# Kernel tuning notes

Hardware: AMD Instinct MI355X
Metric: run time of the kernel (lower is better)

The kernel has to match this reference:

```python
import jax, jax.numpy as jnp
import numpy as np

N_NODES = 100000
N_EDGES = 1600000
IN, HID, OUT = 128, 128, 64


def setup_inputs() -> dict:
    key = jax.random.key(0)
    ks = jax.random.split(key, 12)
    x = jax.random.normal(ks[0], (N_NODES, IN), dtype=jnp.float32)
    src = jax.random.randint(ks[1], (N_EDGES,), 0, N_NODES, dtype=jnp.int32)
    dst = jax.random.randint(ks[2], (N_EDGES,), 0, N_NODES, dtype=jnp.int32)
    def lin(k, fan_in, fan_out):
        s = 1.0 / np.sqrt(fan_in)
        return (jax.random.normal(k, (fan_in, fan_out), dtype=jnp.float32) * s)
    dims = [(IN, HID), (HID, HID), (HID, OUT)]
    params = {}
    for l, (fi, fo) in enumerate(dims):
        params[f"Wself{l}"] = lin(ks[3 + 3 * l], fi, fo)
        params[f"Wneigh{l}"] = lin(ks[4 + 3 * l], fi, fo)
        params[f"b{l}"] = jnp.zeros((fo,), dtype=jnp.float32)
    return {"x": x, "src": src, "dst": dst, **params}


def _sage_conv(h, src, dst, inv_deg, Ws, Wn, b):
    # mean aggregation over in-neighbors: segment-sum of gathered src feats / degree
    agg = jax.ops.segment_sum(h[src], dst, num_segments=N_NODES) * inv_deg
    return h @ Ws + agg @ Wn + b


def reference(x, src, dst, Wself0, Wneigh0, b0, Wself1, Wneigh1, b1, Wself2, Wneigh2, b2):
    deg = jax.ops.segment_sum(jnp.ones((N_EDGES,), jnp.float32), dst, num_segments=N_NODES)
    inv_deg = (1.0 / jnp.maximum(deg, 1.0))[:, None]  # zero-degree nodes get zero agg
    h = jax.nn.relu(_sage_conv(x, src, dst, inv_deg, Wself0, Wneigh0, b0))
    h = jax.nn.relu(_sage_conv(h, src, dst, inv_deg, Wself1, Wneigh1, b1))
    h = _sage_conv(h, src, dst, inv_deg, Wself2, Wneigh2, b2)
    return h
```

## Files before the change

kernel.cpp:

```cpp
#include <hip/hip_runtime.h>
#include <hip/hip_bf16.h>

#define N_NODES 100000
#define N_EDGES 1600000
#define BSHIFT 8
#define NB 391
#define BCAP 8192

typedef __attribute__((ext_vector_type(8))) short short8;
typedef __attribute__((ext_vector_type(4))) float f32x4;
typedef unsigned short ushort;
typedef unsigned int uint;

__device__ __forceinline__ ushort f2bf(float f) {
    uint u = __float_as_uint(f);
    uint r = (u + 0x7fffu + ((u >> 16) & 1u)) >> 16;
    return (ushort)r;
}
__device__ __forceinline__ float bflo(uint v) { return __uint_as_float(v << 16); }
__device__ __forceinline__ float bfhi(uint v) { return __uint_as_float(v & 0xffff0000u); }


__global__ __launch_bounds__(256) void partA_kernel(const int* __restrict__ src,
                                                    const int* __restrict__ dst,
                                                    uint* __restrict__ packed,
                                                    int* __restrict__ bucket_cnt, int E) {
    constexpr int PER = 16;
    __shared__ int cnt[NB];
    __shared__ int cur[NB];
    int tid = threadIdx.x;
    for (int i = tid; i < NB; i += 256) cnt[i] = 0;
    __syncthreads();
    int base = blockIdx.x * (256 * PER);
    int d[PER], s[PER];
#pragma unroll
    for (int i = 0; i < PER; i++) {
        int e = base + tid + i * 256;
        if (e < E) {
            d[i] = dst[e];
            s[i] = src[e];
            atomicAdd(&cnt[d[i] >> BSHIFT], 1);
        } else {
            d[i] = -1;
        }
    }
    __syncthreads();
    for (int i = tid; i < NB; i += 256) cur[i] = atomicAdd(&bucket_cnt[i], cnt[i]);
    __syncthreads();
#pragma unroll
    for (int i = 0; i < PER; i++) {
        if (d[i] >= 0) {
            int b = d[i] >> BSHIFT;
            int p = atomicAdd(&cur[b], 1);
            packed[(size_t)b * BCAP + p] = ((uint)(d[i] & 255) << 17) | (uint)s[i];
        }
    }
}


__global__ __launch_bounds__(256) void partB_kernel(const uint* __restrict__ packed,
                                                    const int* __restrict__ bucket_cnt,
                                                    int* __restrict__ row_ptr,
                                                    float* __restrict__ inv_deg,
                                                    int* __restrict__ col, int N, int E) {
    __shared__ int deg[256];
    __shared__ int cur[256];
    __shared__ int psum[256];
    __shared__ int sofs;
    int b = blockIdx.x, tid = threadIdx.x;
    int cnt = bucket_cnt[b];
    {
        int part = 0;
        for (int i = tid; i < b; i += 256) part += bucket_cnt[i];
        psum[tid] = part;
        __syncthreads();
        for (int off = 128; off > 0; off >>= 1) {
            if (tid < off) psum[tid] += psum[tid + off];
            __syncthreads();
        }
        if (tid == 0) sofs = psum[0];
        __syncthreads();
    }
    int bofs = sofs;
    const uint* pk = packed + (size_t)b * BCAP;
    deg[tid] = 0;
    __syncthreads();
    for (int e = tid; e < cnt; e += 1024) {
        uint w[4];
        int have[4];
#pragma unroll
        for (int j = 0; j < 4; j++) {
            int ee = e + j * 256;
            have[j] = ee < cnt;
            w[j] = pk[have[j] ? ee : e];
        }
#pragma unroll
        for (int j = 0; j < 4; j++)
            if (have[j]) atomicAdd(&deg[w[j] >> 17], 1);
    }
    __syncthreads();
    int d0 = deg[tid];
    psum[tid] = d0;
    __syncthreads();
    for (int off = 1; off < 256; off <<= 1) {
        int x = psum[tid];
        int y = (tid >= off) ? psum[tid - off] : 0;
        __syncthreads();
        psum[tid] = x + y;
        __syncthreads();
    }
    int excl = psum[tid] - d0;
    cur[tid] = excl;
    int g = (b << BSHIFT) + tid;
    if (g < N) {
        row_ptr[g] = bofs + excl;
        inv_deg[g] = 1.0f / (float)(d0 > 1 ? d0 : 1);
    }
    if (b == 0 && tid == 0) row_ptr[N] = E;
    __syncthreads();
    for (int e = tid; e < cnt; e += 1024) {
        uint w[4];
        int have[4];
#pragma unroll
        for (int j = 0; j < 4; j++) {
            int ee = e + j * 256;
            have[j] = ee < cnt;
            w[j] = pk[have[j] ? ee : e];
        }
#pragma unroll
        for (int j = 0; j < 4; j++)
            if (have[j]) {
                int dl = w[j] >> 17;
                int p = atomicAdd(&cur[dl], 1);
                col[bofs + p] = (int)(w[j] & 0x1FFFFu);
            }
    }
}


#define CAST_BLK 6250

__global__ __launch_bounds__(256) void prep_kernel(const float* __restrict__ x,
                                                   ushort* __restrict__ xb,
                                                   const float* __restrict__ Ws0,
                                                   const float* __restrict__ Wn0,
                                                   const float* __restrict__ Ws1,
                                                   const float* __restrict__ Wn1,
                                                   const float* __restrict__ Ws2,
                                                   const float* __restrict__ Wn2,
                                                   ushort* __restrict__ BT0,
                                                   ushort* __restrict__ BT1,
                                                   ushort* __restrict__ BT2) {
    int blk = blockIdx.x;
    if (blk < CAST_BLK) {
        long n8 = (long)N_NODES * 128 / 8;
        long g = (long)blk * 256 + threadIdx.x;
        if (g >= n8) return;
        const float4* x4 = (const float4*)x;
        float4 a = x4[g * 2], b = x4[g * 2 + 1];
        uint4 o;
        o.x = (uint)f2bf(a.x) | ((uint)f2bf(a.y) << 16);
        o.y = (uint)f2bf(a.z) | ((uint)f2bf(a.w) << 16);
        o.z = (uint)f2bf(b.x) | ((uint)f2bf(b.y) << 16);
        o.w = (uint)f2bf(b.z) | ((uint)f2bf(b.w) << 16);
        ((uint4*)xb)[g] = o;
        return;
    }
    int idx = (blk - CAST_BLK) * 256 + threadIdx.x;
    const float* Ws;
    const float* Wn;
    ushort* BT;
    int FOUT;
    if (idx < 128 * 256) {
        Ws = Ws0; Wn = Wn0; BT = BT0; FOUT = 128;
    } else if (idx < 2 * 128 * 256) {
        idx -= 128 * 256;
        Ws = Ws1; Wn = Wn1; BT = BT1; FOUT = 128;
    } else if (idx < 2 * 128 * 256 + 64 * 256) {
        idx -= 2 * 128 * 256;
        Ws = Ws2; Wn = Wn2; BT = BT2; FOUT = 64;
    } else {
        return;
    }
    int n = idx >> 8, k = idx & 255;
    float v = (k < 128) ? Ws[k * FOUT + n] : Wn[(k - 128) * FOUT + n];
    BT[idx] = f2bf(v);
}


__global__ __launch_bounds__(256) void agg_kernel(const ushort* __restrict__ hb,
                                                  const int* __restrict__ row_ptr,
                                                  const int* __restrict__ col,
                                                  const float* __restrict__ inv_deg,
                                                  ushort* __restrict__ aggb, int n) {
    int node = (int)((blockIdx.x * blockDim.x + threadIdx.x) >> 6);
    int lane = threadIdx.x & 63;
    if (node >= n) return;
    int quad = lane >> 4;
    int sub = lane & 15;
    const char* hbase = (const char*)hb;
    int beg = row_ptr[node], end = row_ptr[node + 1];
    float acc[8];
#pragma unroll
    for (int j = 0; j < 8; j++) acc[j] = 0.f;
    int suboff = sub * 16;
    for (int e0 = beg; e0 < end; e0 += 16) {
        int rem = end - e0;
        int idxv[4];
        float msk[4];
#pragma unroll
        for (int j = 0; j < 4; j++) {
            int i = quad + 4 * j;
            msk[j] = (i < rem) ? 1.f : 0.f;
            idxv[j] = col[e0 + ((i < rem) ? i : 0)];
        }
        uint4 v[4];
#pragma unroll
        for (int j = 0; j < 4; j++)
            v[j] = *(const uint4*)(hbase + (((uint)idxv[j] << 8) + suboff));
#pragma unroll
        for (int j = 0; j < 4; j++) {
            acc[0] += bflo(v[j].x) * msk[j]; acc[1] += bfhi(v[j].x) * msk[j];
            acc[2] += bflo(v[j].y) * msk[j]; acc[3] += bfhi(v[j].y) * msk[j];
            acc[4] += bflo(v[j].z) * msk[j]; acc[5] += bfhi(v[j].z) * msk[j];
            acc[6] += bflo(v[j].w) * msk[j]; acc[7] += bfhi(v[j].w) * msk[j];
        }
    }
#pragma unroll
    for (int j = 0; j < 8; j++) {
        acc[j] += __shfl_xor(acc[j], 16);
        acc[j] += __shfl_xor(acc[j], 32);
    }
    if (quad == 0) {
        float inv = inv_deg[node];
        uint4 o;
        o.x = (uint)f2bf(acc[0] * inv) | ((uint)f2bf(acc[1] * inv) << 16);
        o.y = (uint)f2bf(acc[2] * inv) | ((uint)f2bf(acc[3] * inv) << 16);
        o.z = (uint)f2bf(acc[4] * inv) | ((uint)f2bf(acc[5] * inv) << 16);
        o.w = (uint)f2bf(acc[6] * inv) | ((uint)f2bf(acc[7] * inv) << 16);
        *(uint4*)((char*)aggb + (size_t)node * 256 + suboff) = o;
    }
}


template <int FOUT, bool RELU, bool OUTBF16>
__global__ __launch_bounds__(256) void mfma_gemm(const ushort* __restrict__ hb,
                                                 const ushort* __restrict__ aggb,
                                                 const ushort* __restrict__ BTb,
                                                 const float* __restrict__ bias,
                                                 void* __restrict__ outp, int nNodes) {
    constexpr int NT = FOUT / 16;
    constexpr int BSTR = 40;
    __shared__ ushort BT[FOUT * BSTR];
    int tid = threadIdx.x;
    int wave = tid >> 6, lane = tid & 63;
    int m = lane & 15, quad = lane >> 4;
    int r0 = blockIdx.x * 64 + wave * 16;
    int arow = r0 + m;
    if (arow >= nNodes) arow = nNodes - 1;
    const ushort* hrow = hb + (size_t)arow * 128;
    const ushort* grow = aggb + (size_t)arow * 128;

    f32x4 acc[NT];
#pragma unroll
    for (int t = 0; t < NT; t++) acc[t] = (f32x4){0.f, 0.f, 0.f, 0.f};

#pragma unroll
    for (int kc = 0; kc < 8; kc++) {
        __syncthreads();
        constexpr int UNITS = FOUT * 4;
#pragma unroll
        for (int u0 = 0; u0 < UNITS / 256; u0++) {
            int u = tid + u0 * 256;
            int n = u >> 2, ko = (u & 3) * 8;
            short8 v = *(const short8*)(BTb + n * 256 + kc * 32 + ko);
            *(short8*)(&BT[n * BSTR + ko]) = v;
        }
        __syncthreads();
        int kg = kc * 32 + quad * 8;
        const ushort* ap = (kg < 128) ? (hrow + kg) : (grow + (kg - 128));
        short8 afrag = *(const short8*)ap;
#pragma unroll
        for (int t = 0; t < NT; t++) {
            short8 bfrag = *(const short8*)(&BT[(t * 16 + m) * BSTR + quad * 8]);
            acc[t] = __builtin_amdgcn_mfma_f32_16x16x32_bf16(afrag, bfrag, acc[t], 0, 0, 0);
        }
    }

#pragma unroll
    for (int reg = 0; reg < 4; reg++) {
        int orow = r0 + quad * 4 + reg;
        if (orow < nNodes) {
#pragma unroll
            for (int t = 0; t < NT; t++) {
                int j = t * 16 + m;
                float v = acc[t][reg] + bias[j];
                if (RELU) v = fmaxf(v, 0.f);
                if (OUTBF16)
                    ((ushort*)outp)[(size_t)orow * FOUT + j] = f2bf(v);
                else
                    ((float*)outp)[(size_t)orow * FOUT + j] = v;
            }
        }
    }
}

extern "C" void kernel_launch(void* const* d_in, const int* in_sizes, int n_in,
                              void* d_out, int out_size, void* d_ws, size_t ws_size,
                              hipStream_t stream) {
    const float* x   = (const float*)d_in[0];
    const int* src   = (const int*)d_in[1];
    const int* dst   = (const int*)d_in[2];
    const float* Ws0 = (const float*)d_in[3];
    const float* Wn0 = (const float*)d_in[4];
    const float* b0  = (const float*)d_in[5];
    const float* Ws1 = (const float*)d_in[6];
    const float* Wn1 = (const float*)d_in[7];
    const float* b1  = (const float*)d_in[8];
    const float* Ws2 = (const float*)d_in[9];
    const float* Wn2 = (const float*)d_in[10];
    const float* b2  = (const float*)d_in[11];
    float* out = (float*)d_out;

    const int N = N_NODES, E = N_EDGES;

    char* p = (char*)d_ws;
    auto take = [&](size_t bytes) {
        void* r = (void*)p;
        p += (bytes + 255) & ~(size_t)255;
        return r;
    };
    uint* packed    = (uint*)take((size_t)NB * BCAP * 4);
    int* bucket_cnt = (int*)take((size_t)NB * 4);
    int* row_ptr    = (int*)take((size_t)(N + 1) * 4);
    int* col        = (int*)take((size_t)E * 4);
    float* inv_deg  = (float*)take((size_t)N * 4);
    ushort* xb      = (ushort*)take((size_t)N * 128 * 2);
    ushort* h1b     = (ushort*)take((size_t)N * 128 * 2);
    ushort* aggb    = (ushort*)take((size_t)N * 128 * 2);
    ushort* BT0     = (ushort*)take((size_t)128 * 256 * 2);
    ushort* BT1     = (ushort*)take((size_t)128 * 256 * 2);
    ushort* BT2     = (ushort*)take((size_t)64 * 256 * 2);

    hipMemsetAsync(bucket_cnt, 0, (size_t)NB * 4, stream);
    int nblkA = (E + 4096 - 1) / 4096;
    partA_kernel<<<nblkA, 256, 0, stream>>>(src, dst, packed, bucket_cnt, E);
    partB_kernel<<<NB, 256, 0, stream>>>(packed, bucket_cnt, row_ptr, inv_deg, col, N, E);

    prep_kernel<<<CAST_BLK + 320, 256, 0, stream>>>(x, xb, Ws0, Wn0, Ws1, Wn1, Ws2, Wn2,
                                                    BT0, BT1, BT2);

    int aggGrid = (int)(((long)N * 64 + 255) / 256);
    int gemmGrid = (N + 63) / 64;

    agg_kernel<<<aggGrid, 256, 0, stream>>>(xb, row_ptr, col, inv_deg, aggb, N);
    mfma_gemm<128, true, true><<<gemmGrid, 256, 0, stream>>>(xb, aggb, BT0, b0, h1b, N);
    agg_kernel<<<aggGrid, 256, 0, stream>>>(h1b, row_ptr, col, inv_deg, aggb, N);
    mfma_gemm<128, true, true><<<gemmGrid, 256, 0, stream>>>(h1b, aggb, BT1, b1, xb, N);
    agg_kernel<<<aggGrid, 256, 0, stream>>>(xb, row_ptr, col, inv_deg, aggb, N);
    mfma_gemm<64, false, false><<<gemmGrid, 256, 0, stream>>>(xb, aggb, BT2, b2, out, N);
}
```

Measured before the change: 389.8 us.

## Fuse neighbor aggregation into GEMM kernel via shared-memory AGG tile

Merges the per-layer aggregation kernel into the MFMA GEMM kernel. Each wave aggregates its 16 rows sequentially into a shared-memory tile, and the GEMM reads the neighbor half of A from that tile. This removes the global aggb write and read and three kernel launches per forward pass. In exchange, parallelism drops: each wave now serially processes 16 nodes instead of one wave per node, so there is less memory-level parallelism for the gather. It also caches packed edge words in registers (KE=20) in partB so the bucket is read once instead of twice.

```diff
diff --git a/kernel.cpp b/kernel.cpp
--- a/kernel.cpp
+++ b/kernel.cpp
@@ -57,6 +57,8 @@
     }
 }
 
+
+#define KE 20
 
 __global__ __launch_bounds__(256) void partB_kernel(const uint* __restrict__ packed,
                                                     const int* __restrict__ bucket_cnt,
@@ -85,19 +87,17 @@
     const uint* pk = packed + (size_t)b * BCAP;
     deg[tid] = 0;
     __syncthreads();
-    for (int e = tid; e < cnt; e += 1024) {
-        uint w[4];
-        int have[4];
-#pragma unroll
-        for (int j = 0; j < 4; j++) {
-            int ee = e + j * 256;
-            have[j] = ee < cnt;
-            w[j] = pk[have[j] ? ee : e];
-        }
-#pragma unroll
-        for (int j = 0; j < 4; j++)
-            if (have[j]) atomicAdd(&deg[w[j] >> 17], 1);
-    }
+    uint w[KE];
+#pragma unroll
+    for (int j = 0; j < KE; j++) {
+        int ee = tid + j * 256;
+        if (ee < cnt) {
+            w[j] = pk[ee];
+            atomicAdd(&deg[w[j] >> 17], 1);
+        }
+    }
+    for (int ee = tid + KE * 256; ee < cnt; ee += 256)
+        atomicAdd(&deg[pk[ee] >> 17], 1);
     __syncthreads();
     int d0 = deg[tid];
     psum[tid] = d0;
@@ -118,22 +118,18 @@
     }
     if (b == 0 && tid == 0) row_ptr[N] = E;
     __syncthreads();
-    for (int e = tid; e < cnt; e += 1024) {
-        uint w[4];
-        int have[4];
-#pragma unroll
-        for (int j = 0; j < 4; j++) {
-            int ee = e + j * 256;
-            have[j] = ee < cnt;
-            w[j] = pk[have[j] ? ee : e];
-        }
-#pragma unroll
-        for (int j = 0; j < 4; j++)
-            if (have[j]) {
-                int dl = w[j] >> 17;
-                int p = atomicAdd(&cur[dl], 1);
-                col[bofs + p] = (int)(w[j] & 0x1FFFFu);
-            }
+#pragma unroll
+    for (int j = 0; j < KE; j++) {
+        int ee = tid + j * 256;
+        if (ee < cnt) {
+            int p = atomicAdd(&cur[w[j] >> 17], 1);
+            col[bofs + p] = (int)(w[j] & 0x1FFFFu);
+        }
+    }
+    for (int ee = tid + KE * 256; ee < cnt; ee += 256) {
+        uint ww = pk[ee];
+        int p = atomicAdd(&cur[ww >> 17], 1);
+        col[bofs + p] = (int)(ww & 0x1FFFFu);
     }
 }
 
@@ -188,78 +184,77 @@
 }
 
 
-__global__ __launch_bounds__(256) void agg_kernel(const ushort* __restrict__ hb,
-                                                  const int* __restrict__ row_ptr,
-                                                  const int* __restrict__ col,
-                                                  const float* __restrict__ inv_deg,
-                                                  ushort* __restrict__ aggb, int n) {
-    int node = (int)((blockIdx.x * blockDim.x + threadIdx.x) >> 6);
-    int lane = threadIdx.x & 63;
-    if (node >= n) return;
-    int quad = lane >> 4;
-    int sub = lane & 15;
-    const char* hbase = (const char*)hb;
-    int beg = row_ptr[node], end = row_ptr[node + 1];
-    float acc[8];
-#pragma unroll
-    for (int j = 0; j < 8; j++) acc[j] = 0.f;
-    int suboff = sub * 16;
-    for (int e0 = beg; e0 < end; e0 += 16) {
-        int rem = end - e0;
-        int idxv[4];
-        float msk[4];
-#pragma unroll
-        for (int j = 0; j < 4; j++) {
-            int i = quad + 4 * j;
-            msk[j] = (i < rem) ? 1.f : 0.f;
-            idxv[j] = col[e0 + ((i < rem) ? i : 0)];
-        }
-        uint4 v[4];
-#pragma unroll
-        for (int j = 0; j < 4; j++)
-            v[j] = *(const uint4*)(hbase + (((uint)idxv[j] << 8) + suboff));
-#pragma unroll
-        for (int j = 0; j < 4; j++) {
-            acc[0] += bflo(v[j].x) * msk[j]; acc[1] += bfhi(v[j].x) * msk[j];
-            acc[2] += bflo(v[j].y) * msk[j]; acc[3] += bfhi(v[j].y) * msk[j];
-            acc[4] += bflo(v[j].z) * msk[j]; acc[5] += bfhi(v[j].z) * msk[j];
-            acc[6] += bflo(v[j].w) * msk[j]; acc[7] += bfhi(v[j].w) * msk[j];
-        }
-    }
-#pragma unroll
-    for (int j = 0; j < 8; j++) {
-        acc[j] += __shfl_xor(acc[j], 16);
-        acc[j] += __shfl_xor(acc[j], 32);
-    }
-    if (quad == 0) {
-        float inv = inv_deg[node];
-        uint4 o;
-        o.x = (uint)f2bf(acc[0] * inv) | ((uint)f2bf(acc[1] * inv) << 16);
-        o.y = (uint)f2bf(acc[2] * inv) | ((uint)f2bf(acc[3] * inv) << 16);
-        o.z = (uint)f2bf(acc[4] * inv) | ((uint)f2bf(acc[5] * inv) << 16);
-        o.w = (uint)f2bf(acc[6] * inv) | ((uint)f2bf(acc[7] * inv) << 16);
-        *(uint4*)((char*)aggb + (size_t)node * 256 + suboff) = o;
-    }
-}
-
+#define ASTR 136
 
 template <int FOUT, bool RELU, bool OUTBF16>
-__global__ __launch_bounds__(256) void mfma_gemm(const ushort* __restrict__ hb,
-                                                 const ushort* __restrict__ aggb,
-                                                 const ushort* __restrict__ BTb,
-                                                 const float* __restrict__ bias,
-                                                 void* __restrict__ outp, int nNodes) {
+__global__ __launch_bounds__(256) void fused_layer(const ushort* __restrict__ hb,
+                                                   const int* __restrict__ row_ptr,
+                                                   const int* __restrict__ col,
+                                                   const float* __restrict__ inv_deg,
+                                                   const ushort* __restrict__ BTb,
+                                                   const float* __restrict__ bias,
+                                                   void* __restrict__ outp, int nNodes) {
     constexpr int NT = FOUT / 16;
     constexpr int BSTR = 40;
     __shared__ ushort BT[FOUT * BSTR];
+    __shared__ ushort AGG[64 * ASTR];
     int tid = threadIdx.x;
     int wave = tid >> 6, lane = tid & 63;
-    int m = lane & 15, quad = lane >> 4;
+    int quad = lane >> 4, sub = lane & 15;
+    int suboff = sub * 16;
+    const char* hbase = (const char*)hb;
     int r0 = blockIdx.x * 64 + wave * 16;
+
+    for (int i = 0; i < 16; i++) {
+        int node = r0 + i;
+        if (node >= nNodes) node = nNodes - 1;
+        int beg = row_ptr[node], end = row_ptr[node + 1];
+        float acc[8];
+#pragma unroll
+        for (int j = 0; j < 8; j++) acc[j] = 0.f;
+        for (int e0 = beg; e0 < end; e0 += 16) {
+            int rem = end - e0;
+            int idxv[4];
+            float msk[4];
+#pragma unroll
+            for (int j = 0; j < 4; j++) {
+                int ii = quad + 4 * j;
+                msk[j] = (ii < rem) ? 1.f : 0.f;
+                idxv[j] = col[e0 + ((ii < rem) ? ii : 0)];
+            }
+            uint4 v[4];
+#pragma unroll
+            for (int j = 0; j < 4; j++)
+                v[j] = *(const uint4*)(hbase + (((uint)idxv[j] << 8) + suboff));
+#pragma unroll
+            for (int j = 0; j < 4; j++) {
+                acc[0] += bflo(v[j].x) * msk[j]; acc[1] += bfhi(v[j].x) * msk[j];
+                acc[2] += bflo(v[j].y) * msk[j]; acc[3] += bfhi(v[j].y) * msk[j];
+                acc[4] += bflo(v[j].z) * msk[j]; acc[5] += bfhi(v[j].z) * msk[j];
+                acc[6] += bflo(v[j].w) * msk[j]; acc[7] += bfhi(v[j].w) * msk[j];
+            }
+        }
+#pragma unroll
+        for (int j = 0; j < 8; j++) {
+            acc[j] += __shfl_xor(acc[j], 16);
+            acc[j] += __shfl_xor(acc[j], 32);
+        }
+        if (quad == 0) {
+            float inv = inv_deg[node];
+            uint4 o;
+            o.x = (uint)f2bf(acc[0] * inv) | ((uint)f2bf(acc[1] * inv) << 16);
+            o.y = (uint)f2bf(acc[2] * inv) | ((uint)f2bf(acc[3] * inv) << 16);
+            o.z = (uint)f2bf(acc[4] * inv) | ((uint)f2bf(acc[5] * inv) << 16);
+            o.w = (uint)f2bf(acc[6] * inv) | ((uint)f2bf(acc[7] * inv) << 16);
+            *(uint4*)&AGG[(wave * 16 + i) * ASTR + sub * 8] = o;
+        }
+    }
+    __syncthreads();
+
+    int m = lane & 15;
     int arow = r0 + m;
     if (arow >= nNodes) arow = nNodes - 1;
     const ushort* hrow = hb + (size_t)arow * 128;
-    const ushort* grow = aggb + (size_t)arow * 128;
 
     f32x4 acc[NT];
 #pragma unroll
@@ -277,9 +272,12 @@
             *(short8*)(&BT[n * BSTR + ko]) = v;
         }
         __syncthreads();
-        int kg = kc * 32 + quad * 8;
-        const ushort* ap = (kg < 128) ? (hrow + kg) : (grow + (kg - 128));
-        short8 afrag = *(const short8*)ap;
+        short8 afrag;
+        if (kc < 4) {
+            afrag = *(const short8*)(hrow + kc * 32 + quad * 8);
+        } else {
+            afrag = *(const short8*)(&AGG[(wave * 16 + m) * ASTR + (kc - 4) * 32 + quad * 8]);
+        }
 #pragma unroll
         for (int t = 0; t < NT; t++) {
             short8 bfrag = *(const short8*)(&BT[(t * 16 + m) * BSTR + quad * 8]);
@@ -337,7 +335,6 @@
     float* inv_deg  = (float*)take((size_t)N * 4);
     ushort* xb      = (ushort*)take((size_t)N * 128 * 2);
     ushort* h1b     = (ushort*)take((size_t)N * 128 * 2);
-    ushort* aggb    = (ushort*)take((size_t)N * 128 * 2);
     ushort* BT0     = (ushort*)take((size_t)128 * 256 * 2);
     ushort* BT1     = (ushort*)take((size_t)128 * 256 * 2);
     ushort* BT2     = (ushort*)take((size_t)64 * 256 * 2);
@@ -350,13 +347,12 @@
     prep_kernel<<<CAST_BLK + 320, 256, 0, stream>>>(x, xb, Ws0, Wn0, Ws1, Wn1, Ws2, Wn2,
                                                     BT0, BT1, BT2);
 
-    int aggGrid = (int)(((long)N * 64 + 255) / 256);
-    int gemmGrid = (N + 63) / 64;
-
-    agg_kernel<<<aggGrid, 256, 0, stream>>>(xb, row_ptr, col, inv_deg, aggb, N);
-    mfma_gemm<128, true, true><<<gemmGrid, 256, 0, stream>>>(xb, aggb, BT0, b0, h1b, N);
-    agg_kernel<<<aggGrid, 256, 0, stream>>>(h1b, row_ptr, col, inv_deg, aggb, N);
-    mfma_gemm<128, true, true><<<gemmGrid, 256, 0, stream>>>(h1b, aggb, BT1, b1, xb, N);
-    agg_kernel<<<aggGrid, 256, 0, stream>>>(xb, row_ptr, col, inv_deg, aggb, N);
-    mfma_gemm<64, false, false><<<gemmGrid, 256, 0, stream>>>(xb, aggb, BT2, b2, out, N);
-}
+    int grid = (N + 63) / 64;
+
+    fused_layer<128, true, true><<<grid, 256, 0, stream>>>(xb, row_ptr, col, inv_deg,
+                                                           BT0, b0, h1b, N);
+    fused_layer<128, true, true><<<grid, 256, 0, stream>>>(h1b, row_ptr, col, inv_deg,
+                                                           BT1, b1, xb, N);
+    fused_layer<64, false, false><<<grid, 256, 0, stream>>>(xb, row_ptr, col, inv_deg,
+                                                            BT2, b2, out, N);
+}
```

Measured after the change: 420.4 us. +7.8%, slower.
